# Performance work log

Hardware: AMD Instinct MI355X
Metric: run time of the kernel (lower is better)

Reference implementation:

```python
import jax, jax.numpy as jnp
import numpy as np

BN_EPS = 1e-5


def setup_inputs() -> dict:
    key = jax.random.key(0)
    ks = jax.random.split(key, 10)
    B, L, V, D = 4096, 200, 100000, 256
    tokens = jax.random.randint(ks[0], (B, L), 0, V, dtype=jnp.int32)
    lengths = jnp.maximum(jax.random.randint(ks[1], (B,), 0, L + 1, dtype=jnp.int32), 1)
    t = (jax.random.uniform(ks[2], (B,)) > 0.5).astype(jnp.float32)
    emb_table = jax.random.normal(ks[3], (V, D), dtype=jnp.float32)
    W1 = jax.random.normal(ks[4], (D, D), dtype=jnp.float32) * (1.0 / np.sqrt(D))
    b1 = jnp.zeros((D,), dtype=jnp.float32)
    gamma = jnp.ones((D,), dtype=jnp.float32)
    beta = jnp.zeros((D,), dtype=jnp.float32)
    w2 = jax.random.normal(ks[5], (D,), dtype=jnp.float32) * (1.0 / np.sqrt(D))
    b2 = jnp.zeros((), dtype=jnp.float32)
    return {"tokens": tokens, "lengths": lengths, "t": t, "emb_table": emb_table,
            "W1": W1, "b1": b1, "gamma": gamma, "beta": beta, "w2": w2, "b2": b2}


def reference(tokens, lengths, t, emb_table, W1, b1, gamma, beta, w2, b2):
    B, L = tokens.shape
    # ragged gather + mean pool (EmbeddingBag-mean equivalent)
    emb = emb_table[tokens]                                   # [B, L, D]
    mask = (jnp.arange(L)[None, :] < lengths[:, None]).astype(emb.dtype)  # [B, L]
    pooled = jnp.einsum('bld,bl->bd', emb, mask) / lengths[:, None].astype(emb.dtype)
    # fc_hidden -> BatchNorm1d (training-mode batch stats) -> ReLU (dropout = eval identity)
    z = pooled @ W1.T + b1                                    # [B, D]
    mu = jnp.mean(z, axis=0)
    var = jnp.var(z, axis=0)
    zn = (z - mu) / jnp.sqrt(var + BN_EPS)
    h = jax.nn.relu(gamma * zn + beta)
    # fc_output -> logits
    logits = h @ w2 + b2                                      # [B]
    # BCEWithLogitsLoss (mean, numerically stable)
    loss = jnp.mean(jnp.maximum(logits, 0.0) - logits * t + jnp.log1p(jnp.exp(-jnp.abs(logits))))
    return (loss, logits)
```

## Files before the change

kernel.cpp:

```cpp
#include <hip/hip_runtime.h>
#include <math.h>

#define L_ 200

__device__ __forceinline__ unsigned f2bf_pair(float a, float b) {
  union { float f; unsigned u; } ca, cb;
  ca.f = a; cb.f = b;
  unsigned ra = (ca.u + 0x7FFFu + ((ca.u >> 16) & 1u)) >> 16;
  unsigned rb = (cb.u + 0x7FFFu + ((cb.u >> 16) & 1u)) >> 16;
  return (ra & 0xFFFFu) | ((rb & 0xFFFFu) << 16);
}

__device__ __forceinline__ float bf_lo(unsigned u) {
  union { unsigned u; float f; } c; c.u = u << 16; return c.f;
}
__device__ __forceinline__ float bf_hi(unsigned u) {
  union { unsigned u; float f; } c; c.u = u & 0xFFFF0000u; return c.f;
}

__global__ __launch_bounds__(256) void convert_pack_kernel(
    const float* __restrict__ emb, uint2* __restrict__ embbf,
    const float* __restrict__ W1, float* __restrict__ W1p,
    float* __restrict__ ssum, float* __restrict__ ssq, float* __restrict__ out) {
  const int tid = threadIdx.x;
  if (blockIdx.x < 64) {
    float4 v = ((const float4*)W1)[tid * 64 + blockIdx.x];
    ((float4*)W1p)[blockIdx.x * 256 + tid] = v;
  } else if (blockIdx.x == 64) {
    ssum[tid] = 0.f;
    ssq[tid] = 0.f;
    if (tid == 0) out[0] = 0.f;
  }
  const float4* e4 = (const float4*)emb;
  const unsigned N4 = 100000u * 64u;
  for (unsigned i = blockIdx.x * 256 + tid; i < N4; i += 2048u * 256u) {
    float4 v = e4[i];
    uint2 o;
    o.x = f2bf_pair(v.x, v.y);
    o.y = f2bf_pair(v.z, v.w);
    embbf[i] = o;
  }
}

__global__ __launch_bounds__(256) void pool_kernel(
    const int* __restrict__ tokens, const int* __restrict__ lengths,
    const uint2* __restrict__ embbf, float* __restrict__ pooled) {
  const int tid = threadIdx.x;
  const int wv = tid >> 6, lane = tid & 63;
  const int row = blockIdx.x * 2 + (wv >> 1);
  const int half = wv & 1;
  const int len = lengths[row];
  const int* trow = tokens + row * L_;
  float4 a0 = make_float4(0.f, 0.f, 0.f, 0.f);
  float4 a1 = a0, a2 = a0, a3 = a0;
  for (int l0 = half * 64; l0 < len; l0 += 128) {
    int nt = len - l0; nt = nt > 64 ? 64 : nt;
    int tk = (lane < nt) ? trow[l0 + lane] : 0;
    int j = 0;
    for (; j + 4 <= nt; j += 4) {
      int t0 = __shfl(tk, j);
      int t1 = __shfl(tk, j + 1);
      int t2 = __shfl(tk, j + 2);
      int t3 = __shfl(tk, j + 3);
      uint2 v0 = embbf[(size_t)t0 * 64 + lane];
      uint2 v1 = embbf[(size_t)t1 * 64 + lane];
      uint2 v2 = embbf[(size_t)t2 * 64 + lane];
      uint2 v3 = embbf[(size_t)t3 * 64 + lane];
      a0.x += bf_lo(v0.x); a0.y += bf_hi(v0.x); a0.z += bf_lo(v0.y); a0.w += bf_hi(v0.y);
      a1.x += bf_lo(v1.x); a1.y += bf_hi(v1.x); a1.z += bf_lo(v1.y); a1.w += bf_hi(v1.y);
      a2.x += bf_lo(v2.x); a2.y += bf_hi(v2.x); a2.z += bf_lo(v2.y); a2.w += bf_hi(v2.y);
      a3.x += bf_lo(v3.x); a3.y += bf_hi(v3.x); a3.z += bf_lo(v3.y); a3.w += bf_hi(v3.y);
    }
    for (; j < nt; j++) {
      int t0 = __shfl(tk, j);
      uint2 v0 = embbf[(size_t)t0 * 64 + lane];
      a0.x += bf_lo(v0.x); a0.y += bf_hi(v0.x); a0.z += bf_lo(v0.y); a0.w += bf_hi(v0.y);
    }
  }
  float4 r;
  r.x = a0.x + a1.x + a2.x + a3.x;
  r.y = a0.y + a1.y + a2.y + a3.y;
  r.z = a0.z + a1.z + a2.z + a3.z;
  r.w = a0.w + a1.w + a2.w + a3.w;
  __shared__ float4 part[2][64];
  if (half) part[wv >> 1][lane] = r;
  __syncthreads();
  if (!half) {
    float4 o = part[wv >> 1][lane];
    const float inv = 1.0f / (float)len;
    r.x = (r.x + o.x) * inv;
    r.y = (r.y + o.y) * inv;
    r.z = (r.z + o.z) * inv;
    r.w = (r.w + o.w) * inv;
    ((float4*)pooled)[(size_t)row * 64 + lane] = r;
  }
}

__global__ __launch_bounds__(256) void gemm_stats_kernel(
    const float* __restrict__ pooled, const float* __restrict__ W1p,
    const float* __restrict__ b1, float* __restrict__ z,
    float* __restrict__ ssum, float* __restrict__ ssq) {
  __shared__ float4 SH[1024];
  const int tid = threadIdx.x;
  const int b0 = blockIdx.x * 16;
  const float4* pooled4 = (const float4*)pooled;
#pragma unroll
  for (int i = 0; i < 4; i++)
    SH[tid + i * 256] = pooled4[(size_t)b0 * 64 + tid + i * 256];
  __syncthreads();
  const int wv = tid >> 6, lane = tid & 63;
  const int r0 = wv * 4;
  float4 bb = ((const float4*)b1)[lane];
  float acc[4][4];
#pragma unroll
  for (int r = 0; r < 4; r++) {
    acc[r][0] = bb.x; acc[r][1] = bb.y; acc[r][2] = bb.z; acc[r][3] = bb.w;
  }
  const float4* w4 = (const float4*)W1p;
  for (int kb = 0; kb < 64; kb++) {
    float4 wk0 = w4[kb * 256 + lane * 4 + 0];
    float4 wk1 = w4[kb * 256 + lane * 4 + 1];
    float4 wk2 = w4[kb * 256 + lane * 4 + 2];
    float4 wk3 = w4[kb * 256 + lane * 4 + 3];
#pragma unroll
    for (int r = 0; r < 4; r++) {
      float4 p = SH[(r0 + r) * 64 + kb];
      acc[r][0] += p.x * wk0.x + p.y * wk0.y + p.z * wk0.z + p.w * wk0.w;
      acc[r][1] += p.x * wk1.x + p.y * wk1.y + p.z * wk1.z + p.w * wk1.w;
      acc[r][2] += p.x * wk2.x + p.y * wk2.y + p.z * wk2.z + p.w * wk2.w;
      acc[r][3] += p.x * wk3.x + p.y * wk3.y + p.z * wk3.z + p.w * wk3.w;
    }
  }
  float4* z4 = (float4*)z;
  float4 s = make_float4(0.f, 0.f, 0.f, 0.f), q = s;
#pragma unroll
  for (int r = 0; r < 4; r++) {
    float4 o = make_float4(acc[r][0], acc[r][1], acc[r][2], acc[r][3]);
    z4[(size_t)(b0 + r0 + r) * 64 + lane] = o;
    s.x += o.x; s.y += o.y; s.z += o.z; s.w += o.w;
    q.x += o.x * o.x; q.y += o.y * o.y; q.z += o.z * o.z; q.w += o.w * o.w;
  }
  __syncthreads();
  SH[wv * 64 + lane] = s;
  SH[256 + wv * 64 + lane] = q;
  __syncthreads();
  if (tid < 64) {
    float4 S = make_float4(0.f, 0.f, 0.f, 0.f), Q = S;
#pragma unroll
    for (int w = 0; w < 4; w++) {
      float4 a = SH[w * 64 + tid];
      float4 b = SH[256 + w * 64 + tid];
      S.x += a.x; S.y += a.y; S.z += a.z; S.w += a.w;
      Q.x += b.x; Q.y += b.y; Q.z += b.z; Q.w += b.w;
    }
    atomicAdd(&ssum[4 * tid + 0], S.x);
    atomicAdd(&ssum[4 * tid + 1], S.y);
    atomicAdd(&ssum[4 * tid + 2], S.z);
    atomicAdd(&ssum[4 * tid + 3], S.w);
    atomicAdd(&ssq[4 * tid + 0], Q.x);
    atomicAdd(&ssq[4 * tid + 1], Q.y);
    atomicAdd(&ssq[4 * tid + 2], Q.z);
    atomicAdd(&ssq[4 * tid + 3], Q.w);
  }
}

__global__ __launch_bounds__(256) void head_loss_kernel(
    const float* __restrict__ z, const float* __restrict__ ssum,
    const float* __restrict__ ssq, const float* __restrict__ gamma,
    const float* __restrict__ beta, const float* __restrict__ w2,
    const float* __restrict__ b2, const float* __restrict__ t,
    float* __restrict__ out) {
  const int tid = threadIdx.x;
  const int wv = tid >> 6, lane = tid & 63;
  const int b = blockIdx.x * 4 + wv;
  float4 s4 = ((const float4*)ssum)[lane];
  float4 q4 = ((const float4*)ssq)[lane];
  float4 g4 = ((const float4*)gamma)[lane];
  float4 be4 = ((const float4*)beta)[lane];
  float4 w24 = ((const float4*)w2)[lane];
  const float invB = 1.0f / 4096.0f;
  float4 A4, C4;
  {
    float m = s4.x * invB, v = q4.x * invB - m * m;
    float rs = rsqrtf(v + 1e-5f); A4.x = g4.x * rs; C4.x = be4.x - m * A4.x;
  }
  {
    float m = s4.y * invB, v = q4.y * invB - m * m;
    float rs = rsqrtf(v + 1e-5f); A4.y = g4.y * rs; C4.y = be4.y - m * A4.y;
  }
  {
    float m = s4.z * invB, v = q4.z * invB - m * m;
    float rs = rsqrtf(v + 1e-5f); A4.z = g4.z * rs; C4.z = be4.z - m * A4.z;
  }
  {
    float m = s4.w * invB, v = q4.w * invB - m * m;
    float rs = rsqrtf(v + 1e-5f); A4.w = g4.w * rs; C4.w = be4.w - m * A4.w;
  }
  float4 zv = ((const float4*)z)[(size_t)b * 64 + lane];
  float h0 = fmaxf(A4.x * zv.x + C4.x, 0.f);
  float h1 = fmaxf(A4.y * zv.y + C4.y, 0.f);
  float h2 = fmaxf(A4.z * zv.z + C4.z, 0.f);
  float h3 = fmaxf(A4.w * zv.w + C4.w, 0.f);
  float part = h0 * w24.x + h1 * w24.y + h2 * w24.z + h3 * w24.w;
#pragma unroll
  for (int off = 32; off > 0; off >>= 1) part += __shfl_down(part, off);
  __shared__ float red[4];
  if (lane == 0) {
    float logit = part + b2[0];
    out[1 + b] = logit;
    float tb = t[b];
    red[wv] = fmaxf(logit, 0.f) - logit * tb + log1pf(expf(-fabsf(logit)));
  }
  __syncthreads();
  if (tid == 0)
    atomicAdd(out, (red[0] + red[1] + red[2] + red[3]) * (1.0f / 4096.0f));
}

extern "C" void kernel_launch(void* const* d_in, const int* in_sizes, int n_in,
                              void* d_out, int out_size, void* d_ws, size_t ws_size,
                              hipStream_t stream) {
  const int* tokens = (const int*)d_in[0];
  const int* lengths = (const int*)d_in[1];
  const float* t = (const float*)d_in[2];
  const float* emb = (const float*)d_in[3];
  const float* W1 = (const float*)d_in[4];
  const float* b1 = (const float*)d_in[5];
  const float* gamma = (const float*)d_in[6];
  const float* beta = (const float*)d_in[7];
  const float* w2 = (const float*)d_in[8];
  const float* b2 = (const float*)d_in[9];
  float* out = (float*)d_out;

  float* wsf = (float*)d_ws;
  uint2* embbf = (uint2*)d_ws;
  float* pooled = wsf + 12800000;
  float* z = wsf + 13848576;
  float* W1p = wsf + 14897152;
  float* ssum = wsf + 14962688;
  float* ssq = wsf + 14962944;

  convert_pack_kernel<<<2048, 256, 0, stream>>>(emb, embbf, W1, W1p, ssum, ssq, out);
  pool_kernel<<<2048, 256, 0, stream>>>(tokens, lengths, embbf, pooled);
  gemm_stats_kernel<<<256, 256, 0, stream>>>(pooled, W1p, b1, z, ssum, ssq);
  head_loss_kernel<<<1024, 256, 0, stream>>>(z, ssum, ssq, gamma, beta, w2, b2, t, out);
}
```

Baseline: 280.7 us.

## Gather fp32 embeddings directly and fuse packing into the pooling kernel

Removes the per-call pass that converts the whole 100k x 256 embedding table to bf16. The pooling kernel now gathers fp32 rows directly and also does the W1 repacking and statistics zeroing, so one launch is dropped. The gather loop is unrolled to 8 tokens per step to keep more loads in flight. In exchange, each gathered row is twice as many bytes as with bf16, so performance depends on how much of the random gather is served from cache. Accumulation precision also improves, since rows are no longer rounded to bf16.

```diff
diff --git a/kernel.cpp b/kernel.cpp
--- a/kernel.cpp
+++ b/kernel.cpp
@@ -3,23 +3,9 @@
 
 #define L_ 200
 
-__device__ __forceinline__ unsigned f2bf_pair(float a, float b) {
-  union { float f; unsigned u; } ca, cb;
-  ca.f = a; cb.f = b;
-  unsigned ra = (ca.u + 0x7FFFu + ((ca.u >> 16) & 1u)) >> 16;
-  unsigned rb = (cb.u + 0x7FFFu + ((cb.u >> 16) & 1u)) >> 16;
-  return (ra & 0xFFFFu) | ((rb & 0xFFFFu) << 16);
-}
-
-__device__ __forceinline__ float bf_lo(unsigned u) {
-  union { unsigned u; float f; } c; c.u = u << 16; return c.f;
-}
-__device__ __forceinline__ float bf_hi(unsigned u) {
-  union { unsigned u; float f; } c; c.u = u & 0xFFFF0000u; return c.f;
-}
-
-__global__ __launch_bounds__(256) void convert_pack_kernel(
-    const float* __restrict__ emb, uint2* __restrict__ embbf,
+__global__ __launch_bounds__(256) void pool_pack_kernel(
+    const int* __restrict__ tokens, const int* __restrict__ lengths,
+    const float* __restrict__ emb, float* __restrict__ pooled,
     const float* __restrict__ W1, float* __restrict__ W1p,
     float* __restrict__ ssum, float* __restrict__ ssq, float* __restrict__ out) {
   const int tid = threadIdx.x;
@@ -31,50 +17,44 @@
     ssq[tid] = 0.f;
     if (tid == 0) out[0] = 0.f;
   }
-  const float4* e4 = (const float4*)emb;
-  const unsigned N4 = 100000u * 64u;
-  for (unsigned i = blockIdx.x * 256 + tid; i < N4; i += 2048u * 256u) {
-    float4 v = e4[i];
-    uint2 o;
-    o.x = f2bf_pair(v.x, v.y);
-    o.y = f2bf_pair(v.z, v.w);
-    embbf[i] = o;
-  }
-}
-
-__global__ __launch_bounds__(256) void pool_kernel(
-    const int* __restrict__ tokens, const int* __restrict__ lengths,
-    const uint2* __restrict__ embbf, float* __restrict__ pooled) {
-  const int tid = threadIdx.x;
   const int wv = tid >> 6, lane = tid & 63;
   const int row = blockIdx.x * 2 + (wv >> 1);
   const int half = wv & 1;
   const int len = lengths[row];
   const int* trow = tokens + row * L_;
+  const float4* embv = (const float4*)emb;
   float4 a0 = make_float4(0.f, 0.f, 0.f, 0.f);
   float4 a1 = a0, a2 = a0, a3 = a0;
   for (int l0 = half * 64; l0 < len; l0 += 128) {
     int nt = len - l0; nt = nt > 64 ? 64 : nt;
     int tk = (lane < nt) ? trow[l0 + lane] : 0;
     int j = 0;
-    for (; j + 4 <= nt; j += 4) {
+    for (; j + 8 <= nt; j += 8) {
       int t0 = __shfl(tk, j);
       int t1 = __shfl(tk, j + 1);
       int t2 = __shfl(tk, j + 2);
       int t3 = __shfl(tk, j + 3);
-      uint2 v0 = embbf[(size_t)t0 * 64 + lane];
-      uint2 v1 = embbf[(size_t)t1 * 64 + lane];
-      uint2 v2 = embbf[(size_t)t2 * 64 + lane];
-      uint2 v3 = embbf[(size_t)t3 * 64 + lane];
-      a0.x += bf_lo(v0.x); a0.y += bf_hi(v0.x); a0.z += bf_lo(v0.y); a0.w += bf_hi(v0.y);
-      a1.x += bf_lo(v1.x); a1.y += bf_hi(v1.x); a1.z += bf_lo(v1.y); a1.w += bf_hi(v1.y);
-      a2.x += bf_lo(v2.x); a2.y += bf_hi(v2.x); a2.z += bf_lo(v2.y); a2.w += bf_hi(v2.y);
-      a3.x += bf_lo(v3.x); a3.y += bf_hi(v3.x); a3.z += bf_lo(v3.y); a3.w += bf_hi(v3.y);
+      int t4 = __shfl(tk, j + 4);
+      int t5 = __shfl(tk, j + 5);
+      int t6 = __shfl(tk, j + 6);
+      int t7 = __shfl(tk, j + 7);
+      float4 v0 = embv[(size_t)t0 * 64 + lane];
+      float4 v1 = embv[(size_t)t1 * 64 + lane];
+      float4 v2 = embv[(size_t)t2 * 64 + lane];
+      float4 v3 = embv[(size_t)t3 * 64 + lane];
+      float4 v4 = embv[(size_t)t4 * 64 + lane];
+      float4 v5 = embv[(size_t)t5 * 64 + lane];
+      float4 v6 = embv[(size_t)t6 * 64 + lane];
+      float4 v7 = embv[(size_t)t7 * 64 + lane];
+      a0.x += v0.x + v4.x; a0.y += v0.y + v4.y; a0.z += v0.z + v4.z; a0.w += v0.w + v4.w;
+      a1.x += v1.x + v5.x; a1.y += v1.y + v5.y; a1.z += v1.z + v5.z; a1.w += v1.w + v5.w;
+      a2.x += v2.x + v6.x; a2.y += v2.y + v6.y; a2.z += v2.z + v6.z; a2.w += v2.w + v6.w;
+      a3.x += v3.x + v7.x; a3.y += v3.y + v7.y; a3.z += v3.z + v7.z; a3.w += v3.w + v7.w;
     }
     for (; j < nt; j++) {
       int t0 = __shfl(tk, j);
-      uint2 v0 = embbf[(size_t)t0 * 64 + lane];
-      a0.x += bf_lo(v0.x); a0.y += bf_hi(v0.x); a0.z += bf_lo(v0.y); a0.w += bf_hi(v0.y);
+      float4 v0 = embv[(size_t)t0 * 64 + lane];
+      a0.x += v0.x; a0.y += v0.y; a0.z += v0.z; a0.w += v0.w;
     }
   }
   float4 r;
@@ -232,15 +212,14 @@
   float* out = (float*)d_out;
 
   float* wsf = (float*)d_ws;
-  uint2* embbf = (uint2*)d_ws;
-  float* pooled = wsf + 12800000;
-  float* z = wsf + 13848576;
-  float* W1p = wsf + 14897152;
-  float* ssum = wsf + 14962688;
-  float* ssq = wsf + 14962944;
-
-  convert_pack_kernel<<<2048, 256, 0, stream>>>(emb, embbf, W1, W1p, ssum, ssq, out);
-  pool_kernel<<<2048, 256, 0, stream>>>(tokens, lengths, embbf, pooled);
+  float* pooled = wsf;
+  float* z = wsf + 1048576;
+  float* W1p = wsf + 2097152;
+  float* ssum = wsf + 2162688;
+  float* ssq = wsf + 2162944;
+
+  pool_pack_kernel<<<2048, 256, 0, stream>>>(tokens, lengths, emb, pooled,
+                                             W1, W1p, ssum, ssq, out);
   gemm_stats_kernel<<<256, 256, 0, stream>>>(pooled, W1p, b1, z, ssum, ssq);
   head_loss_kernel<<<1024, 256, 0, stream>>>(z, ssum, ssq, gamma, beta, w2, b2, t, out);
 }
```

Measured after the change: 271.5 us. 3.3% less time.
